# Optimization experiments

Measured on AMD Instinct MI355X. Metric: run time of the kernel, lower is better.

## Reference

```python
import jax, jax.numpy as jnp
import numpy as np

N_FULL, N_SUB, NNZ = 100000, 32768, 1048576
F_IN, DH, DOUT = 512, 512, 512
EPS_NORM = 1e-9   # HighOrderAggregator 'norm' bias eps
EPS_L2 = 1e-12    # F.normalize eps


def spmm(row, col, val, feat, n):
    # sparse [n,n] @ dense [n,d] via gather + segment-sum scatter
    return jax.ops.segment_sum(val[:, None] * feat[col], row, num_segments=n)


def ho_layer(row, col, val, feat, Ws, bs, scales, offsets, n):
    # HighOrderAggregator, order=1, act=relu, bias='norm', aggr='concat'
    hops = [feat, spmm(row, col, val, feat, n)]
    parts = []
    for h, W, b, s, o in zip(hops, Ws, bs, scales, offsets):
        f = jax.nn.relu(h @ W.T + b)
        mean = jnp.mean(f, axis=1, keepdims=True)
        var = jnp.var(f, axis=1, keepdims=True)  # unbiased=False, matches torch
        parts.append((f - mean) * s * jax.lax.rsqrt(var + EPS_NORM) + o)
    return jnp.concatenate(parts, axis=1)


def _xavier(k, shape):
    fan_out, fan_in = shape
    lim = float(np.sqrt(6.0 / (fan_in + fan_out)))
    return jax.random.uniform(k, shape, jnp.float32, -lim, lim)


def setup_inputs() -> dict:
    key = jax.random.key(0)
    ks = jax.random.split(key, 24)
    inp = {}
    inp['feat_full'] = jax.random.normal(ks[0], (N_FULL, F_IN), jnp.float32)
    inp['node_subgraph'] = jax.random.randint(ks[1], (N_SUB,), 0, N_FULL)
    inp['adj_row'] = jax.random.randint(ks[2], (NNZ,), 0, N_SUB)
    inp['adj_col'] = jax.random.randint(ks[3], (NNZ,), 0, N_SUB)
    inp['adj_val'] = jax.random.uniform(ks[4], (NNZ,), jnp.float32)
    # layer 1: dim_in=512 -> 512 per order, concat -> 1024
    inp['W1_0'] = _xavier(ks[5], (DH, F_IN))
    inp['W1_1'] = _xavier(ks[6], (DH, F_IN))
    inp['b1_0'] = 0.02 * jax.random.normal(ks[7], (DH,), jnp.float32)
    inp['b1_1'] = 0.02 * jax.random.normal(ks[8], (DH,), jnp.float32)
    inp['s1_0'] = 1.0 + 0.1 * jax.random.normal(ks[9], (DH,), jnp.float32)
    inp['s1_1'] = 1.0 + 0.1 * jax.random.normal(ks[10], (DH,), jnp.float32)
    inp['o1_0'] = 0.02 * jax.random.normal(ks[11], (DH,), jnp.float32)
    inp['o1_1'] = 0.02 * jax.random.normal(ks[12], (DH,), jnp.float32)
    # layer 2: dim_in=1024 -> 512 per order, concat -> 1024
    inp['W2_0'] = _xavier(ks[13], (DH, 2 * DH))
    inp['W2_1'] = _xavier(ks[14], (DH, 2 * DH))
    inp['b2_0'] = 0.02 * jax.random.normal(ks[15], (DH,), jnp.float32)
    inp['b2_1'] = 0.02 * jax.random.normal(ks[16], (DH,), jnp.float32)
    inp['s2_0'] = 1.0 + 0.1 * jax.random.normal(ks[17], (DH,), jnp.float32)
    inp['s2_1'] = 1.0 + 0.1 * jax.random.normal(ks[18], (DH,), jnp.float32)
    inp['o2_0'] = 0.02 * jax.random.normal(ks[19], (DH,), jnp.float32)
    inp['o2_1'] = 0.02 * jax.random.normal(ks[20], (DH,), jnp.float32)
    # classifier: order=0, act='I', bias='bias'
    inp['Wc'] = _xavier(ks[21], (DOUT, 2 * DH))
    inp['bc'] = 0.02 * jax.random.normal(ks[22], (DOUT,), jnp.float32)
    return inp


def reference(feat_full, node_subgraph, adj_row, adj_col, adj_val,
              W1_0, W1_1, b1_0, b1_1, s1_0, s1_1, o1_0, o1_1,
              W2_0, W2_1, b2_0, b2_1, s2_0, s2_1, o2_0, o2_1,
              Wc, bc):
    feat = feat_full[node_subgraph]                       # [N_SUB, F_IN] gather
    h = ho_layer(adj_row, adj_col, adj_val, feat,
                 (W1_0, W1_1), (b1_0, b1_1), (s1_0, s1_1), (o1_0, o1_1), N_SUB)
    h = ho_layer(adj_row, adj_col, adj_val, h,
                 (W2_0, W2_1), (b2_0, b2_1), (s2_0, s2_1), (o2_0, o2_1), N_SUB)
    nrm = jnp.linalg.norm(h, axis=1, keepdims=True)       # F.normalize p=2 dim=1
    h = h / jnp.maximum(nrm, EPS_L2)
    return h @ Wc.T + bc                                  # classifier (act='I')
```

## Files before the change

kernel.cpp:

```cpp
#include <hip/hip_runtime.h>
#include <stdint.h>

typedef unsigned short u16;
typedef unsigned int u32;

#define NSUB 32768
#define NNZ_E 1048576

using short8 = __attribute__((ext_vector_type(8))) short;
using f32x4  = __attribute__((ext_vector_type(4))) float;

__device__ __forceinline__ u16 f2b(float f) {
  u32 u = __float_as_uint(f);
  return (u16)((u + 0x7fffu + ((u >> 16) & 1u)) >> 16);
}
__device__ __forceinline__ float b2f(u16 x) {
  return __uint_as_float(((u32)x) << 16);
}

__device__ __forceinline__ void glds16(const void* g, void* l) {
  __builtin_amdgcn_global_load_lds(
      (const __attribute__((address_space(1))) u32*)g,
      (__attribute__((address_space(3))) u32*)l, 16, 0, 0);
}

#define GATHER_B 16384
#define COUNT_B 4096
__global__ __launch_bounds__(256) void u_prep(
    const float* __restrict__ ff, const int* __restrict__ idx, u16* __restrict__ FEAT,
    const int* __restrict__ arow, const int* __restrict__ acol, int* __restrict__ cnt8,
    const float* W1_0, const float* W1_1, const float* W2_0, const float* W2_1,
    const float* Wc, u16* W1_0b, u16* W1_1b, u16* W2cat, u16* Wcb) {
  int bid = blockIdx.x, t = threadIdx.x;
  if (bid < GATHER_B) {
    int r = bid * 2 + (t >> 7);
    int c = (t & 127) * 4;
    size_t src = (size_t)idx[r];
    float4 v = *(const float4*)(ff + src * 512 + c);
    ushort4 o;
    o.x = f2b(v.x); o.y = f2b(v.y); o.z = f2b(v.z); o.w = f2b(v.w);
    *(ushort4*)(FEAT + (size_t)r * 512 + c) = o;
  } else if (bid < GATHER_B + COUNT_B) {
    int i = (bid - GATHER_B) * 256 + t;
    atomicAdd(&cnt8[arow[i] * 8 + (acol[i] >> 12)], 1);
  } else {
    int cid = bid - GATHER_B - COUNT_B;
    const float* src; u16* dst; int i;
    if (cid < 256)       { src = W1_0; dst = W1_0b;              i = cid * 256 + t; }
    else if (cid < 512)  { src = W1_1; dst = W1_1b;              i = (cid - 256) * 256 + t; }
    else if (cid < 1024) { src = W2_0; dst = W2cat;              i = (cid - 512) * 256 + t; }
    else if (cid < 1536) { src = W2_1; dst = W2cat + 512 * 1024; i = (cid - 1024) * 256 + t; }
    else                 { src = Wc;   dst = Wcb;                i = (cid - 1536) * 256 + t; }
    float4 v = ((const float4*)src)[i];
    ushort4 o;
    o.x = f2b(v.x); o.y = f2b(v.y); o.z = f2b(v.z); o.w = f2b(v.w);
    ((ushort4*)dst)[i] = o;
  }
}

__global__ __launch_bounds__(256) void scan_part(const int* __restrict__ cnt8,
                                                 int* __restrict__ bsum) {
  int bid = blockIdx.x, t = threadIdx.x;
  int4 c = *(const int4*)(cnt8 + bid * 1024 + t * 4);
  int s = c.x + c.y + c.z + c.w;
#pragma unroll
  for (int d = 1; d < 64; d <<= 1) s += __shfl_xor(s, d);
  __shared__ int red[4];
  if ((t & 63) == 0) red[t >> 6] = s;
  __syncthreads();
  if (t == 0) bsum[bid] = red[0] + red[1] + red[2] + red[3];
}

__global__ __launch_bounds__(256) void scan_top(const int* __restrict__ bsum,
                                                int* __restrict__ boff) {
  int t = threadIdx.x;
  int v = bsum[t];
  int s = v;
#pragma unroll
  for (int d = 1; d < 64; d <<= 1) {
    int u = __shfl_up(s, d);
    if ((t & 63) >= d) s += u;
  }
  __shared__ int wsum[4];
  if ((t & 63) == 63) wsum[t >> 6] = s;
  __syncthreads();
  int add = 0;
  for (int w = 0; w < (t >> 6); ++w) add += wsum[w];
  boff[t] = s + add - v;
}

__global__ __launch_bounds__(256) void scan_final(const int* __restrict__ cnt8,
                                                  const int* __restrict__ boff,
                                                  int* __restrict__ off,
                                                  int* __restrict__ cursor8) {
  int bid = blockIdx.x, t = threadIdx.x;
  int base = bid * 1024 + t * 4;
  int4 c = *(const int4*)(cnt8 + base);
  int s = c.x + c.y + c.z + c.w;
  int inc = s;
#pragma unroll
  for (int d = 1; d < 64; d <<= 1) {
    int u = __shfl_up(inc, d);
    if ((t & 63) >= d) inc += u;
  }
  __shared__ int wsum[4];
  if ((t & 63) == 63) wsum[t >> 6] = inc;
  __syncthreads();
  int add = 0;
  for (int w = 0; w < (t >> 6); ++w) add += wsum[w];
  int run = boff[bid] + inc + add - s;
  int vals[4] = {c.x, c.y, c.z, c.w};
#pragma unroll
  for (int j = 0; j < 4; ++j) {
    int idx = base + j;
    cursor8[idx] = run;
    if ((idx & 7) == 0) off[idx >> 3] = run;
    run += vals[j];
  }
  if (bid == 255 && t == 255) off[NSUB] = run;
}

__global__ __launch_bounds__(256) void edge_scatter8(const int* __restrict__ row,
                                                     const int* __restrict__ col,
                                                     const float* __restrict__ val,
                                                     int* __restrict__ cursor8,
                                                     int2* __restrict__ cv) {
  int i = blockIdx.x * 256 + threadIdx.x;
  int c = col[i];
  int p = atomicAdd(&cursor8[row[i] * 8 + (c >> 12)], 1);
  int2 e; e.x = c; e.y = __float_as_int(val[i]);
  cv[p] = e;
}

__device__ __forceinline__ void norm_rowstore(float* a, int lane, int r,
                                              const float* __restrict__ bias,
                                              const float* __restrict__ sc,
                                              const float* __restrict__ ofs,
                                              u16* __restrict__ Y, int ldy, int col_off) {
  float4 b0 = *(const float4*)(bias + lane * 8);
  float4 b1 = *(const float4*)(bias + lane * 8 + 4);
  a[0] = fmaxf(a[0] + b0.x, 0.f); a[1] = fmaxf(a[1] + b0.y, 0.f);
  a[2] = fmaxf(a[2] + b0.z, 0.f); a[3] = fmaxf(a[3] + b0.w, 0.f);
  a[4] = fmaxf(a[4] + b1.x, 0.f); a[5] = fmaxf(a[5] + b1.y, 0.f);
  a[6] = fmaxf(a[6] + b1.z, 0.f); a[7] = fmaxf(a[7] + b1.w, 0.f);
  float sum = 0.f, sq = 0.f;
#pragma unroll
  for (int j = 0; j < 8; ++j) { sum += a[j]; sq += a[j] * a[j]; }
#pragma unroll
  for (int d = 1; d < 64; d <<= 1) {
    sum += __shfl_xor(sum, d);
    sq  += __shfl_xor(sq, d);
  }
  float mean = sum * (1.f / 512.f);
  float var = sq * (1.f / 512.f) - mean * mean;
  float rstd = rsqrtf(var + 1e-9f);
  float4 s0 = *(const float4*)(sc + lane * 8);
  float4 s1 = *(const float4*)(sc + lane * 8 + 4);
  float4 o0 = *(const float4*)(ofs + lane * 8);
  float4 o1 = *(const float4*)(ofs + lane * 8 + 4);
  int4 o;
  o.x = (int)((u32)f2b((a[0] - mean) * s0.x * rstd + o0.x) |
              ((u32)f2b((a[1] - mean) * s0.y * rstd + o0.y) << 16));
  o.y = (int)((u32)f2b((a[2] - mean) * s0.z * rstd + o0.z) |
              ((u32)f2b((a[3] - mean) * s0.w * rstd + o0.w) << 16));
  o.z = (int)((u32)f2b((a[4] - mean) * s1.x * rstd + o1.x) |
              ((u32)f2b((a[5] - mean) * s1.y * rstd + o1.y) << 16));
  o.w = (int)((u32)f2b((a[6] - mean) * s1.z * rstd + o1.z) |
              ((u32)f2b((a[7] - mean) * s1.w * rstd + o1.w) << 16));
  *(int4*)(Y + (size_t)r * ldy + col_off + lane * 8) = o;
}

__device__ __forceinline__ void fma8(int4 u, float v, float* a) {
  u32 w;
  w = (u32)u.x; a[0] += v * __uint_as_float(w << 16); a[1] += v * __uint_as_float(w & 0xffff0000u);
  w = (u32)u.y; a[2] += v * __uint_as_float(w << 16); a[3] += v * __uint_as_float(w & 0xffff0000u);
  w = (u32)u.z; a[4] += v * __uint_as_float(w << 16); a[5] += v * __uint_as_float(w & 0xffff0000u);
  w = (u32)u.w; a[6] += v * __uint_as_float(w << 16); a[7] += v * __uint_as_float(w & 0xffff0000u);
}

template <int LDX, bool NORM>
__device__ __forceinline__ void spmm_dev(const int* __restrict__ off,
                                         const int2* __restrict__ cv,
                                         const u16* __restrict__ X,
                                         u16* __restrict__ Y, int ldy, int col_off,
                                         const float* __restrict__ bias,
                                         const float* __restrict__ sc,
                                         const float* __restrict__ ofs, int bid) {
  const int lane = threadIdx.x & 63, wave = threadIdx.x >> 6;
  const int r = bid * 4 + wave;
  const int s = __builtin_amdgcn_readfirstlane(off[r]);
  const int e = __builtin_amdgcn_readfirstlane(off[r + 1]);
  float a[8] = {0.f, 0.f, 0.f, 0.f, 0.f, 0.f, 0.f, 0.f};
  const u16* Xl = X + lane * 8;
  int i = s;
  for (; i + 4 <= e; i += 4) {
    int2 p0 = cv[i], p1 = cv[i + 1], p2 = cv[i + 2], p3 = cv[i + 3];
    int4 u0 = *(const int4*)(Xl + (size_t)p0.x * LDX);
    int4 u1 = *(const int4*)(Xl + (size_t)p1.x * LDX);
    int4 u2 = *(const int4*)(Xl + (size_t)p2.x * LDX);
    int4 u3 = *(const int4*)(Xl + (size_t)p3.x * LDX);
    fma8(u0, __int_as_float(p0.y), a);
    fma8(u1, __int_as_float(p1.y), a);
    fma8(u2, __int_as_float(p2.y), a);
    fma8(u3, __int_as_float(p3.y), a);
  }
  for (; i < e; ++i) {
    int2 p0 = cv[i];
    int4 u0 = *(const int4*)(Xl + (size_t)p0.x * LDX);
    fma8(u0, __int_as_float(p0.y), a);
  }
  if (NORM) {
    norm_rowstore(a, lane, r, bias, sc, ofs, Y, ldy, col_off);
  } else {
    int4 o;
    o.x = (int)((u32)f2b(a[0]) | ((u32)f2b(a[1]) << 16));
    o.y = (int)((u32)f2b(a[2]) | ((u32)f2b(a[3]) << 16));
    o.z = (int)((u32)f2b(a[4]) | ((u32)f2b(a[5]) << 16));
    o.w = (int)((u32)f2b(a[6]) | ((u32)f2b(a[7]) << 16));
    *(int4*)(Y + (size_t)r * ldy + col_off + lane * 8) = o;
  }
}

__device__ __forceinline__ void rownorm_dev(const u16* __restrict__ F, int ldf,
                                            const float* __restrict__ bias,
                                            const float* __restrict__ sc,
                                            const float* __restrict__ ofs,
                                            u16* __restrict__ Y, int ldy, int col_off,
                                            int bid) {
  const int lane = threadIdx.x & 63, wave = threadIdx.x >> 6;
  const int r = bid * 4 + wave;
  int4 u = *(const int4*)(F + (size_t)r * ldf + lane * 8);
  float a[8];
  a[0] = __uint_as_float(((u32)u.x) << 16); a[1] = __uint_as_float(((u32)u.x) & 0xffff0000u);
  a[2] = __uint_as_float(((u32)u.y) << 16); a[3] = __uint_as_float(((u32)u.y) & 0xffff0000u);
  a[4] = __uint_as_float(((u32)u.z) << 16); a[5] = __uint_as_float(((u32)u.z) & 0xffff0000u);
  a[6] = __uint_as_float(((u32)u.w) << 16); a[7] = __uint_as_float(((u32)u.w) & 0xffff0000u);
  norm_rowstore(a, lane, r, bias, sc, ofs, Y, ldy, col_off);
}

__global__ __launch_bounds__(256) void rownorm_k(const u16* __restrict__ F, int ldf,
                                                 const float* __restrict__ bias,
                                                 const float* __restrict__ sc,
                                                 const float* __restrict__ ofs,
                                                 u16* __restrict__ Y, int col_off) {
  rownorm_dev(F, ldf, bias, sc, ofs, Y, 1024, col_off, blockIdx.x);
}

__global__ __launch_bounds__(256) void u_l1a(const int* __restrict__ row_off,
                                             const int2* __restrict__ cv,
                                             const u16* __restrict__ FEAT,
                                             u16* __restrict__ S1,
                                             const u16* __restrict__ W1_0b,
                                             u16* __restrict__ TMPa) {
  if (blockIdx.x >= 1024) {
    spmm_dev<512, false>(row_off, cv, FEAT, S1, 512, 0, nullptr, nullptr, nullptr,
                         blockIdx.x - 1024);
    return;
  }
  __shared__ __align__(16) u16 As[128 * 32];
  __shared__ __align__(16) u16 Bs[128 * 32];
  const int K = 512, LDC = 512;
  const int t = threadIdx.x;
  const int lane = t & 63, wave = t >> 6;
  const int wm = (wave >> 1) * 64, wn = (wave & 1) * 64;
  const int nwg = 1024;
  const int bid = blockIdx.x;
  const int sbid = (bid % 8) * (nwg / 8) + bid / 8;
  const int bx = sbid % 4, by = sbid / 4;
  const int m0 = by * 128, n0 = bx * 128;

  f32x4 acc[4][4];
#pragma unroll
  for (int m = 0; m < 4; ++m)
#pragma unroll
    for (int n = 0; n < 4; ++n) acc[m][n] = f32x4{0.f, 0.f, 0.f, 0.f};

  const int lr = t >> 2;
  const int lc = (t & 3) * 8;
  const u16* Ag  = FEAT + (size_t)(m0 + lr) * K + lc;
  const u16* Ag2 = Ag + (size_t)64 * K;
  const u16* Wg  = W1_0b + (size_t)(n0 + lr) * K + lc;
  const u16* Wg2 = Wg + (size_t)64 * K;
  char* asb0 = (char*)As + wave * 1024;
  char* asb1 = (char*)As + 4096 + wave * 1024;
  char* bsb0 = (char*)Bs + wave * 1024;
  char* bsb1 = (char*)Bs + 4096 + wave * 1024;
  const int fr = lane & 15, kh = lane >> 4;

  for (int kt = 0; kt < K / 32; ++kt) {
    glds16(Ag + kt * 32, asb0);
    glds16(Ag2 + kt * 32, asb1);
    glds16(Wg + kt * 32, bsb0);
    glds16(Wg2 + kt * 32, bsb1);
    __syncthreads();
    short8 af[4], bfr[4];
#pragma unroll
    for (int m = 0; m < 4; ++m)
      af[m] = *(const short8*)&As[(wm + m * 16 + fr) * 32 + kh * 8];
#pragma unroll
    for (int n = 0; n < 4; ++n)
      bfr[n] = *(const short8*)&Bs[(wn + n * 16 + fr) * 32 + kh * 8];
#pragma unroll
    for (int m = 0; m < 4; ++m)
#pragma unroll
      for (int n = 0; n < 4; ++n)
        acc[m][n] = __builtin_amdgcn_mfma_f32_16x16x32_bf16(af[m], bfr[n], acc[m][n], 0, 0, 0);
    __syncthreads();
  }

  const int crow = (lane >> 4) * 4;
  const int ccol = lane & 15;
#pragma unroll
  for (int n = 0; n < 4; ++n) {
    int col = n0 + wn + n * 16 + ccol;
#pragma unroll
    for (int m = 0; m < 4; ++m) {
      int row = m0 + wm + m * 16 + crow;
#pragma unroll
      for (int q = 0; q < 4; ++q)
        TMPa[(size_t)(row + q) * LDC + col] = f2b(acc[m][n][q]);
    }
  }
}

__global__ __launch_bounds__(256) void u_l2(const int* __restrict__ row_off,
                                            const int2* __restrict__ cv,
                                            const u16* __restrict__ TTL,
                                            u16* __restrict__ H2,
                                            const float* __restrict__ b2_0,
                                            const float* __restrict__ s2_0,
                                            const float* __restrict__ o2_0,
                                            const float* __restrict__ b2_1,
                                            const float* __restrict__ s2_1,
                                            const float* __restrict__ o2_1) {
  int bid = blockIdx.x;
  if (bid < 8192)
    spmm_dev<1024, true>(row_off, cv, TTL + 512, H2, 1024, 512, b2_1, s2_1, o2_1, bid);
  else
    rownorm_dev(TTL, 1024, b2_0, s2_0, o2_0, H2, 1024, 0, bid - 8192);
}

template <int K, int LDC, bool BIAS, bool BF16OUT, bool RS>
__global__ __launch_bounds__(256) void gemm_bt(const u16* __restrict__ A,
                                               const u16* __restrict__ W,
                                               const float* __restrict__ bias,
                                               const float* __restrict__ rs,
                                               float* __restrict__ Cf,
                                               u16* __restrict__ Cb) {
  __shared__ __align__(16) u16 As[128 * 32];
  __shared__ __align__(16) u16 Bs[128 * 32];
  const int t = threadIdx.x;
  const int lane = t & 63, wave = t >> 6;
  const int wm = (wave >> 1) * 64, wn = (wave & 1) * 64;
  const int nwg = gridDim.x * gridDim.y;
  const int bid = blockIdx.x + gridDim.x * blockIdx.y;
  const int sbid = (bid % 8) * (nwg / 8) + bid / 8;
  const int bx = sbid % gridDim.x, by = sbid / gridDim.x;
  const int m0 = by * 128, n0 = bx * 128;

  f32x4 acc[4][4];
#pragma unroll
  for (int m = 0; m < 4; ++m)
#pragma unroll
    for (int n = 0; n < 4; ++n) acc[m][n] = f32x4{0.f, 0.f, 0.f, 0.f};

  const int lr = t >> 2;
  const int lc = (t & 3) * 8;
  const u16* Ag  = A + (size_t)(m0 + lr) * K + lc;
  const u16* Ag2 = Ag + (size_t)64 * K;
  const u16* Wg  = W + (size_t)(n0 + lr) * K + lc;
  const u16* Wg2 = Wg + (size_t)64 * K;
  char* asb0 = (char*)As + wave * 1024;
  char* asb1 = (char*)As + 4096 + wave * 1024;
  char* bsb0 = (char*)Bs + wave * 1024;
  char* bsb1 = (char*)Bs + 4096 + wave * 1024;
  const int fr = lane & 15, kh = lane >> 4;

  for (int kt = 0; kt < K / 32; ++kt) {
    glds16(Ag + kt * 32, asb0);
    glds16(Ag2 + kt * 32, asb1);
    glds16(Wg + kt * 32, bsb0);
    glds16(Wg2 + kt * 32, bsb1);
    __syncthreads();
    short8 af[4], bfr[4];
#pragma unroll
    for (int m = 0; m < 4; ++m)
      af[m] = *(const short8*)&As[(wm + m * 16 + fr) * 32 + kh * 8];
#pragma unroll
    for (int n = 0; n < 4; ++n)
      bfr[n] = *(const short8*)&Bs[(wn + n * 16 + fr) * 32 + kh * 8];
#pragma unroll
    for (int m = 0; m < 4; ++m)
#pragma unroll
      for (int n = 0; n < 4; ++n)
        acc[m][n] = __builtin_amdgcn_mfma_f32_16x16x32_bf16(af[m], bfr[n], acc[m][n], 0, 0, 0);
    __syncthreads();
  }

  const int crow = (lane >> 4) * 4;
  const int ccol = lane & 15;
#pragma unroll
  for (int n = 0; n < 4; ++n) {
    int col = n0 + wn + n * 16 + ccol;
    float bv = BIAS ? bias[col] : 0.f;
#pragma unroll
    for (int m = 0; m < 4; ++m) {
      int row = m0 + wm + m * 16 + crow;
#pragma unroll
      for (int q = 0; q < 4; ++q) {
        float v = acc[m][n][q];
        if (RS) v *= rs[row + q];
        v += bv;
        if (BF16OUT)
          Cb[(size_t)(row + q) * LDC + col] = f2b(v);
        else
          Cf[(size_t)(row + q) * LDC + col] = v;
      }
    }
  }
}

__global__ __launch_bounds__(256) void l2scale(const u16* __restrict__ H,
                                               float* __restrict__ rn) {
  const int lane = threadIdx.x & 63, wave = threadIdx.x >> 6;
  const int r = blockIdx.x * 4 + wave;
  const u16* row = H + (size_t)r * 1024 + lane * 16;
  int4 u0 = *(const int4*)row;
  int4 u1 = *(const int4*)(row + 8);
  float sq = 0.f;
  const int vals[8] = {u0.x, u0.y, u0.z, u0.w, u1.x, u1.y, u1.z, u1.w};
#pragma unroll
  for (int j = 0; j < 8; ++j) {
    u32 wv = (u32)vals[j];
    float f0 = __uint_as_float(wv << 16);
    float f1 = __uint_as_float(wv & 0xffff0000u);
    sq += f0 * f0 + f1 * f1;
  }
#pragma unroll
  for (int d = 1; d < 64; d <<= 1) sq += __shfl_xor(sq, d);
  if (lane == 0) rn[r] = 1.f / fmaxf(sqrtf(sq), 1e-12f);
}

extern "C" void kernel_launch(void* const* d_in, const int* in_sizes, int n_in,
                              void* d_out, int out_size, void* d_ws, size_t ws_size,
                              hipStream_t stream) {
  (void)in_sizes; (void)n_in; (void)out_size; (void)ws_size;
  const float* feat_full = (const float*)d_in[0];
  const int*   nodes = (const int*)d_in[1];
  const int*   arow = (const int*)d_in[2];
  const int*   acol = (const int*)d_in[3];
  const float* aval = (const float*)d_in[4];
  const float* W1_0 = (const float*)d_in[5];
  const float* W1_1 = (const float*)d_in[6];
  const float* b1_0 = (const float*)d_in[7];
  const float* b1_1 = (const float*)d_in[8];
  const float* s1_0 = (const float*)d_in[9];
  const float* s1_1 = (const float*)d_in[10];
  const float* o1_0 = (const float*)d_in[11];
  const float* o1_1 = (const float*)d_in[12];
  const float* W2_0 = (const float*)d_in[13];
  const float* W2_1 = (const float*)d_in[14];
  const float* b2_0 = (const float*)d_in[15];
  const float* b2_1 = (const float*)d_in[16];
  const float* s2_0 = (const float*)d_in[17];
  const float* s2_1 = (const float*)d_in[18];
  const float* o2_0 = (const float*)d_in[19];
  const float* o2_1 = (const float*)d_in[20];
  const float* Wc = (const float*)d_in[21];
  const float* bc = (const float*)d_in[22];
  float* out = (float*)d_out;

  const size_t MB = (size_t)1 << 20;
  char* p = (char*)d_ws;
  u16* FEAT = (u16*)p;
  u16* S1   = (u16*)(p + 32 * MB);
  u16* H1   = (u16*)(p + 64 * MB);
  u16* H2   = (u16*)(p + 128 * MB);
  u16* TMPa = (u16*)(p + 192 * MB);
  u16* TMPb = (u16*)(p + 224 * MB);
  u16* TTL  = (u16*)(p + 192 * MB);
  u16* W1_0b = (u16*)(p + 256 * MB);
  u16* W1_1b = W1_0b + 512 * 512;
  u16* W2cat = W1_1b + 512 * 512;
  u16* Wcb   = W2cat + 1024 * 1024;
  int* row_off = (int*)(p + 260 * MB);
  int* cnt8    = (int*)(p + 261 * MB);
  int* cursor8 = (int*)(p + 262 * MB);
  float* RN    = (float*)(p + 263 * MB);
  int* bsum    = (int*)((char*)RN + 256 * 1024);
  int* boff    = bsum + 256;
  int2* cv     = (int2*)(p + 264 * MB);

  hipMemsetAsync(cnt8, 0, NSUB * 8 * sizeof(int), stream);

  u_prep<<<GATHER_B + COUNT_B + 2048, 256, 0, stream>>>(
      feat_full, nodes, FEAT, arow, acol, cnt8,
      W1_0, W1_1, W2_0, W2_1, Wc, W1_0b, W1_1b, W2cat, Wcb);

  scan_part<<<256, 256, 0, stream>>>(cnt8, bsum);
  scan_top<<<1, 256, 0, stream>>>(bsum, boff);
  scan_final<<<256, 256, 0, stream>>>(cnt8, boff, row_off, cursor8);
  edge_scatter8<<<NNZ_E / 256, 256, 0, stream>>>(arow, acol, aval, cursor8, cv);

  u_l1a<<<1024 + 8192, 256, 0, stream>>>(row_off, cv, FEAT, S1, W1_0b, TMPa);
  gemm_bt<512, 512, false, true, false><<<dim3(4, 256), 256, 0, stream>>>(
      S1, W1_1b, nullptr, nullptr, nullptr, TMPb);
  rownorm_k<<<NSUB / 4, 256, 0, stream>>>(TMPa, 512, b1_0, s1_0, o1_0, H1, 0);
  rownorm_k<<<NSUB / 4, 256, 0, stream>>>(TMPb, 512, b1_1, s1_1, o1_1, H1, 512);

  gemm_bt<1024, 1024, false, true, false><<<dim3(8, 256), 256, 0, stream>>>(
      H1, W2cat, nullptr, nullptr, nullptr, TTL);
  u_l2<<<8192 + 8192, 256, 0, stream>>>(row_off, cv, TTL, H2,
                                        b2_0, s2_0, o2_0, b2_1, s2_1, o2_1);

  l2scale<<<NSUB / 4, 256, 0, stream>>>(H2, RN);
  gemm_bt<1024, 512, true, false, true><<<dim3(4, 256), 256, 0, stream>>>(
      H2, Wcb, bc, RN, out, nullptr);
}
```

Before: 639.1 us.

## Use K=64 swizzled LDS tiles in GEMM and merge layer-1 rownorm launches

The bf16 MFMA GEMM now stages 64-wide K slices per iteration instead of 32, with an XOR swizzle on the LDS layout. This halves the number of barrier pairs per K loop and is meant to avoid LDS bank conflicts on the fragment reads. The two layer-1 row-normalization launches are also merged into one kernel that branches on block index, saving a launch. LDS use per block doubles, which could lower occupancy.

```diff
diff --git a/kernel.cpp b/kernel.cpp
--- a/kernel.cpp
+++ b/kernel.cpp
@@ -238,12 +238,20 @@
   norm_rowstore(a, lane, r, bias, sc, ofs, Y, ldy, col_off);
 }
 
-__global__ __launch_bounds__(256) void rownorm_k(const u16* __restrict__ F, int ldf,
-                                                 const float* __restrict__ bias,
-                                                 const float* __restrict__ sc,
-                                                 const float* __restrict__ ofs,
-                                                 u16* __restrict__ Y, int col_off) {
-  rownorm_dev(F, ldf, bias, sc, ofs, Y, 1024, col_off, blockIdx.x);
+__global__ __launch_bounds__(256) void rownorm2_k(const u16* __restrict__ TMPa,
+                                                  const u16* __restrict__ TMPb,
+                                                  const float* __restrict__ b1_0,
+                                                  const float* __restrict__ s1_0,
+                                                  const float* __restrict__ o1_0,
+                                                  const float* __restrict__ b1_1,
+                                                  const float* __restrict__ s1_1,
+                                                  const float* __restrict__ o1_1,
+                                                  u16* __restrict__ H1) {
+  int bid = blockIdx.x;
+  if (bid < 8192)
+    rownorm_dev(TMPa, 512, b1_0, s1_0, o1_0, H1, 1024, 0, bid);
+  else
+    rownorm_dev(TMPb, 512, b1_1, s1_1, o1_1, H1, 1024, 512, bid - 8192);
 }
 
 __global__ __launch_bounds__(256) void u_l1a(const int* __restrict__ row_off,
@@ -341,14 +349,14 @@
 }
 
 template <int K, int LDC, bool BIAS, bool BF16OUT, bool RS>
-__global__ __launch_bounds__(256) void gemm_bt(const u16* __restrict__ A,
-                                               const u16* __restrict__ W,
-                                               const float* __restrict__ bias,
-                                               const float* __restrict__ rs,
-                                               float* __restrict__ Cf,
-                                               u16* __restrict__ Cb) {
-  __shared__ __align__(16) u16 As[128 * 32];
-  __shared__ __align__(16) u16 Bs[128 * 32];
+__global__ __launch_bounds__(256) void gemm64_bt(const u16* __restrict__ A,
+                                                 const u16* __restrict__ W,
+                                                 const float* __restrict__ bias,
+                                                 const float* __restrict__ rs,
+                                                 float* __restrict__ Cf,
+                                                 u16* __restrict__ Cb) {
+  __shared__ __align__(16) u16 As[128 * 64];
+  __shared__ __align__(16) u16 Bs[128 * 64];
   const int t = threadIdx.x;
   const int lane = t & 63, wave = t >> 6;
   const int wm = (wave >> 1) * 64, wn = (wave & 1) * 64;
@@ -364,36 +372,38 @@
 #pragma unroll
     for (int n = 0; n < 4; ++n) acc[m][n] = f32x4{0.f, 0.f, 0.f, 0.f};
 
-  const int lr = t >> 2;
-  const int lc = (t & 3) * 8;
-  const u16* Ag  = A + (size_t)(m0 + lr) * K + lc;
-  const u16* Ag2 = Ag + (size_t)64 * K;
-  const u16* Wg  = W + (size_t)(n0 + lr) * K + lc;
-  const u16* Wg2 = Wg + (size_t)64 * K;
-  char* asb0 = (char*)As + wave * 1024;
-  char* asb1 = (char*)As + 4096 + wave * 1024;
-  char* bsb0 = (char*)Bs + wave * 1024;
-  char* bsb1 = (char*)Bs + 4096 + wave * 1024;
+  const int sr = t >> 3;
+  const int ss = (t & 7) ^ (sr & 7);
+  const u16* Asrc = A + (size_t)(m0 + sr) * K + ss * 8;
+  const u16* Bsrc = W + (size_t)(n0 + sr) * K + ss * 8;
+  char* adst = (char*)As + wave * 1024;
+  char* bdst = (char*)Bs + wave * 1024;
   const int fr = lane & 15, kh = lane >> 4;
-
-  for (int kt = 0; kt < K / 32; ++kt) {
-    glds16(Ag + kt * 32, asb0);
-    glds16(Ag2 + kt * 32, asb1);
-    glds16(Wg + kt * 32, bsb0);
-    glds16(Wg2 + kt * 32, bsb1);
+  const int sw = fr & 7;
+
+  for (int kt = 0; kt < K / 64; ++kt) {
+#pragma unroll
+    for (int c = 0; c < 4; ++c) {
+      glds16(Asrc + (size_t)(c * 32) * K + kt * 64, adst + c * 4096);
+      glds16(Bsrc + (size_t)(c * 32) * K + kt * 64, bdst + c * 4096);
+    }
     __syncthreads();
-    short8 af[4], bfr[4];
-#pragma unroll
-    for (int m = 0; m < 4; ++m)
-      af[m] = *(const short8*)&As[(wm + m * 16 + fr) * 32 + kh * 8];
-#pragma unroll
-    for (int n = 0; n < 4; ++n)
-      bfr[n] = *(const short8*)&Bs[(wn + n * 16 + fr) * 32 + kh * 8];
-#pragma unroll
-    for (int m = 0; m < 4; ++m)
+#pragma unroll
+    for (int kk = 0; kk < 2; ++kk) {
+      const int so = ((kk * 4 + kh) ^ sw) * 8;
+      short8 af[4], bfr[4];
+#pragma unroll
+      for (int m = 0; m < 4; ++m)
+        af[m] = *(const short8*)&As[(wm + m * 16 + fr) * 64 + so];
 #pragma unroll
       for (int n = 0; n < 4; ++n)
-        acc[m][n] = __builtin_amdgcn_mfma_f32_16x16x32_bf16(af[m], bfr[n], acc[m][n], 0, 0, 0);
+        bfr[n] = *(const short8*)&Bs[(wn + n * 16 + fr) * 64 + so];
+#pragma unroll
+      for (int m = 0; m < 4; ++m)
+#pragma unroll
+        for (int n = 0; n < 4; ++n)
+          acc[m][n] = __builtin_amdgcn_mfma_f32_16x16x32_bf16(af[m], bfr[n], acc[m][n], 0, 0, 0);
+    }
     __syncthreads();
   }
 
@@ -503,17 +513,17 @@
   edge_scatter8<<<NNZ_E / 256, 256, 0, stream>>>(arow, acol, aval, cursor8, cv);
 
   u_l1a<<<1024 + 8192, 256, 0, stream>>>(row_off, cv, FEAT, S1, W1_0b, TMPa);
-  gemm_bt<512, 512, false, true, false><<<dim3(4, 256), 256, 0, stream>>>(
+  gemm64_bt<512, 512, false, true, false><<<dim3(4, 256), 256, 0, stream>>>(
       S1, W1_1b, nullptr, nullptr, nullptr, TMPb);
-  rownorm_k<<<NSUB / 4, 256, 0, stream>>>(TMPa, 512, b1_0, s1_0, o1_0, H1, 0);
-  rownorm_k<<<NSUB / 4, 256, 0, stream>>>(TMPb, 512, b1_1, s1_1, o1_1, H1, 512);
-
-  gemm_bt<1024, 1024, false, true, false><<<dim3(8, 256), 256, 0, stream>>>(
+  rownorm2_k<<<16384, 256, 0, stream>>>(TMPa, TMPb, b1_0, s1_0, o1_0,
+                                        b1_1, s1_1, o1_1, H1);
+
+  gemm64_bt<1024, 1024, false, true, false><<<dim3(8, 256), 256, 0, stream>>>(
       H1, W2cat, nullptr, nullptr, nullptr, TTL);
   u_l2<<<8192 + 8192, 256, 0, stream>>>(row_off, cv, TTL, H2,
                                         b2_0, s2_0, o2_0, b2_1, s2_1, o2_1);
 
   l2scale<<<NSUB / 4, 256, 0, stream>>>(H2, RN);
-  gemm_bt<1024, 512, true, false, true><<<dim3(4, 256), 256, 0, stream>>>(
+  gemm64_bt<1024, 512, true, false, true><<<dim3(4, 256), 256, 0, stream>>>(
       H2, Wcb, bc, RN, out, nullptr);
 }
```

After: 625.6 us. 2.1% less time.
